# Performance work log

Hardware: AMD Instinct MI355X
Metric: run time of the kernel (lower is better)

## Reference

```python
import jax, jax.numpy as jnp
import numpy as np

EMBED_DIM = 528
NUM_HEADS = 8
HEAD_DIM = EMBED_DIM // NUM_HEADS  # 66


def setup_inputs() -> dict:
    key = jax.random.key(0)
    k1, k2, k3, k4, k5 = jax.random.split(key, 5)
    B, D, H, W, C = 1, 16, 16, 16, EMBED_DIM
    s = 1.0 / np.sqrt(C)
    return {
        "x": jax.random.normal(k1, (B, D, H, W, C), dtype=jnp.float32),
        "w_qkv": jax.random.uniform(k2, (3 * C, C), dtype=jnp.float32, minval=-s, maxval=s),
        "b_qkv": jax.random.uniform(k3, (3 * C,), dtype=jnp.float32, minval=-s, maxval=s),
        "w_proj": jax.random.uniform(k4, (C, C), dtype=jnp.float32, minval=-s, maxval=s),
        "b_proj": jax.random.uniform(k5, (C,), dtype=jnp.float32, minval=-s, maxval=s),
    }


def reference(x, w_qkv, b_qkv, w_proj, b_proj):
    B, D, H, W, C = x.shape
    N = D * H * W
    h, hd = NUM_HEADS, HEAD_DIM
    scaling = hd ** (-0.5)

    xt = x.reshape(B, N, C)
    # qkv projection: [B, N, 3C] -> [3, B, h, N, hd]
    qkv = xt @ w_qkv.T + b_qkv
    qkv = qkv.reshape(B, N, 3, h, hd).transpose(2, 0, 3, 1, 4)
    q, k, v = qkv[0], qkv[1], qkv[2]

    # full attention over all D*H*W tokens
    attn = jnp.einsum('bhqd,bhkd->bhqk', q, k) * scaling
    attn = jax.nn.softmax(attn, axis=-1)
    out = jnp.einsum('bhqk,bhkd->bhqd', attn, v)  # [B, h, N, hd]

    out = out.transpose(0, 2, 1, 3).reshape(B, N, h * hd)
    out = out @ w_proj.T + b_proj
    return out.reshape(B, D, H, W, C)
```

## Files before the change

### kernel.cpp

```cpp
#include <hip/hip_runtime.h>

typedef __attribute__((ext_vector_type(8))) short bf16x8;
typedef __attribute__((ext_vector_type(4))) float f32x4;
typedef __attribute__((ext_vector_type(16))) float f32x16;

#define DEV __device__ __forceinline__

static constexpr int N_TOK = 4096;
static constexpr int C     = 528;
static constexpr int NH    = 8;
static constexpr int HD    = 66;
static constexpr int HDP   = 96;
static constexpr int VD96  = 96;
static constexpr int KP    = 544;
static constexpr int NQKV  = 1584;
static constexpr int NQKVP = 1632;

DEV unsigned short f2bf(float f) {
    unsigned int u = __float_as_uint(f);
    u = (u + 0x7fffu + ((u >> 16) & 1u)) >> 16;
    return (unsigned short)u;
}
DEV float bf2f(unsigned short h) { return __uint_as_float(((unsigned int)h) << 16); }
DEV unsigned cvtpk2(float a, float b) {
    unsigned r;
    asm("v_cvt_pk_bf16_f32 %0, %1, %2" : "=v"(r) : "v"(a), "v"(b));
    return r;
}
DEV void plswap(unsigned &a, unsigned &b) {
    asm volatile("v_permlane32_swap_b32 %0, %1" : "+v"(a), "+v"(b));
}

__global__ void k_prep_all(const float* __restrict__ x, const float* __restrict__ w_qkv,
                           const float* __restrict__ w_proj,
                           unsigned short* __restrict__ xb, unsigned short* __restrict__ wqkvb,
                           unsigned short* __restrict__ whi, unsigned short* __restrict__ wlo,
                           unsigned short* __restrict__ qb, unsigned short* __restrict__ kbuf) {
    const int T0 = N_TOK * KP;
    const int T1 = T0 + NQKVP * KP;
    const int T2 = T1 + KP * KP;
    const int T3 = T2 + NH * N_TOK * (HDP - HD);
    for (int idx = blockIdx.x * 256 + threadIdx.x; idx < T3; idx += gridDim.x * 256) {
        if (idx < T0) {
            int n = idx / KP, k = idx - n * KP;
            xb[idx] = (k < C) ? f2bf(x[n * C + k]) : (unsigned short)0;
        } else if (idx < T1) {
            int j = idx - T0;
            int n = j / KP, k = j - n * KP;
            wqkvb[j] = (n < NQKV && k < C) ? f2bf(w_qkv[n * C + k]) : (unsigned short)0;
        } else if (idx < T2) {
            int j = idx - T1;
            int n = j / KP, k = j - n * KP;
            unsigned short hi = 0, lo = 0;
            if (n < C && k < C) {
                float v = w_proj[n * C + k];
                hi = f2bf(v);
                lo = f2bf(v - bf2f(hi));
            }
            whi[j] = hi; wlo[j] = lo;
        } else {
            int j = idx - T2;
            int n = j / 30, p = j - 30 * n;
            size_t a = (size_t)n * HDP + HD + p;
            qb[a] = 0; kbuf[a] = 0;
        }
    }
}

__launch_bounds__(256)
__global__ void k_gemm_qkv(const unsigned short* __restrict__ A,
                           const unsigned short* __restrict__ B,
                           const float* __restrict__ bias,
                           unsigned short* __restrict__ qb, unsigned short* __restrict__ kbuf,
                           unsigned short* __restrict__ vtmp) {
    constexpr int LDA = 40;
    __shared__ unsigned short Al[2][128 * LDA];
    __shared__ unsigned short Bl[2][96 * LDA];
    int tid = threadIdx.x, lane = tid & 63, wid = tid >> 6;
    int m0 = blockIdx.x * 128, n0 = blockIdx.y * 96;
    int wm = (wid >> 1) * 64, wn = (wid & 1) * 48;
    int arow0 = tid >> 2, arow1 = (256 + tid) >> 2, akc = (tid & 3) * 8;
    bool bhave = tid < 128;
    int brow1 = (256 + tid) >> 2;
    f32x4 acc[4][3] = {};
    bf16x8 ra0, ra1, rb0, rb1;

    ra0 = *(const bf16x8*)&A[(size_t)(m0 + arow0) * KP + akc];
    ra1 = *(const bf16x8*)&A[(size_t)(m0 + arow1) * KP + akc];
    rb0 = *(const bf16x8*)&B[(size_t)(n0 + arow0) * KP + akc];
    if (bhave) rb1 = *(const bf16x8*)&B[(size_t)(n0 + brow1) * KP + akc];
    *(bf16x8*)&Al[0][arow0 * LDA + akc] = ra0;
    *(bf16x8*)&Al[0][arow1 * LDA + akc] = ra1;
    *(bf16x8*)&Bl[0][arow0 * LDA + akc] = rb0;
    if (bhave) *(bf16x8*)&Bl[0][brow1 * LDA + akc] = rb1;
    __syncthreads();

    int kk = (lane >> 4) * 8, cc = lane & 15;
    for (int kt = 0; kt < 17; kt++) {
        int cur = kt & 1;
        if (kt < 16) {
            int k0 = (kt + 1) * 32;
            ra0 = *(const bf16x8*)&A[(size_t)(m0 + arow0) * KP + k0 + akc];
            ra1 = *(const bf16x8*)&A[(size_t)(m0 + arow1) * KP + k0 + akc];
            rb0 = *(const bf16x8*)&B[(size_t)(n0 + arow0) * KP + k0 + akc];
            if (bhave) rb1 = *(const bf16x8*)&B[(size_t)(n0 + brow1) * KP + k0 + akc];
        }
        bf16x8 af[4], bfr[3];
#pragma unroll
        for (int mi = 0; mi < 4; mi++) af[mi] = *(const bf16x8*)&Al[cur][(wm + mi * 16 + cc) * LDA + kk];
#pragma unroll
        for (int ni = 0; ni < 3; ni++) bfr[ni] = *(const bf16x8*)&Bl[cur][(wn + ni * 16 + cc) * LDA + kk];
#pragma unroll
        for (int mi = 0; mi < 4; mi++)
#pragma unroll
            for (int ni = 0; ni < 3; ni++)
                acc[mi][ni] = __builtin_amdgcn_mfma_f32_16x16x32_bf16(af[mi], bfr[ni], acc[mi][ni], 0, 0, 0);
        if (kt < 16) {
            int nxt = cur ^ 1;
            *(bf16x8*)&Al[nxt][arow0 * LDA + akc] = ra0;
            *(bf16x8*)&Al[nxt][arow1 * LDA + akc] = ra1;
            *(bf16x8*)&Bl[nxt][arow0 * LDA + akc] = rb0;
            if (bhave) *(bf16x8*)&Bl[nxt][brow1 * LDA + akc] = rb1;
        }
        __syncthreads();
    }
#pragma unroll
    for (int mi = 0; mi < 4; mi++)
#pragma unroll
        for (int ni = 0; ni < 3; ni++)
#pragma unroll
            for (int r = 0; r < 4; r++) {
                int row = m0 + wm + mi * 16 + (lane >> 4) * 4 + r;
                int col = n0 + wn + ni * 16 + cc;
                float v = acc[mi][ni][r] + (col < NQKV ? bias[col] : 0.f);
                unsigned short b = f2bf(v);
                if (col < 2 * C) {
                    int d5 = (col >= C) ? col - C : col;
                    unsigned h = (unsigned)d5 / 66u;
                    int dd = d5 - 66 * (int)h;
                    size_t a = ((size_t)h * N_TOK + row) * HDP + dd;
                    if (col >= C) kbuf[a] = b; else qb[a] = b;
                } else if (col < NQKV) {
                    vtmp[(size_t)row * C + (col - 2 * C)] = b;
                }
            }
}

__global__ void k_reshape_v(const unsigned short* __restrict__ vtmp, unsigned short* __restrict__ vt) {
    __shared__ unsigned short lt[64 * 104];
    int h = blockIdx.y, n0 = blockIdx.x * 64, tid = threadIdx.x;
#pragma unroll
    for (int i = 0; i < 24; i++) {
        int idx = i * 256 + tid;
        int ni = idx / 96, d = idx - ni * 96;
        unsigned short v = 0;
        if (d < HD) v = vtmp[(size_t)(n0 + ni) * C + h * HD + d];
        lt[ni * 104 + d] = v;
    }
    __syncthreads();
#pragma unroll
    for (int i = 0; i < 24; i++) {
        int idx = i * 256 + tid;
        int d = idx >> 6, ni = idx & 63;
        vt[((size_t)h * VD96 + d) * N_TOK + n0 + ni] = lt[ni * 104 + d];
    }
}

__launch_bounds__(512, 2)
__global__ void k_attn(const unsigned short* __restrict__ qb,
                       const unsigned short* __restrict__ kb,
                       const unsigned short* __restrict__ vt,
                       unsigned short* __restrict__ ahi,
                       unsigned short* __restrict__ alo) {
    __shared__ __align__(16) unsigned short S[128 * 128 + 96 * 128];
    int tid = threadIdx.x, lane = tid & 63, wid = tid >> 6;
    int wq = wid & 3;
    int kh = wid >> 2;
    int hi = lane >> 5, lq = lane & 31;
    int bid = blockIdx.x;
    int head = bid & 7;
    int q0 = (bid >> 3) * 128;
    const float SC2 = 0.12309149097933274f * 1.4426950408889634f;

    bf16x8 aq[6];
    {
        const unsigned short* qrow = qb + ((size_t)head * N_TOK + q0 + wq * 32 + lq) * HDP + hi * 8;
#pragma unroll
        for (int t = 0; t < 6; t++) aq[t] = *(const bf16x8*)&qrow[t * 16];
    }
    f32x16 o0 = {}, o1 = {}, o2 = {};
    float m_r = -3e38f, l_r = 0.f;

    const unsigned short* kg = kb + (size_t)head * N_TOK * HDP;
    const unsigned short* vg = vt + (size_t)head * VD96 * N_TOK;

    const unsigned short* gpK[3];
    const unsigned short* gpV[3];
    int laK[3], laV[3];
#pragma unroll
    for (int j = 0; j < 3; j++) {
        int c = j * 512 + tid;
        int row = c / 12, ch = c - row * 12;
        gpK[j] = kg + (size_t)row * HDP + ch * 8;
        laK[j] = row * 128 + ((ch ^ (row & 15)) << 3);
        int row2 = c >> 4, ch2 = c & 15;
        gpV[j] = vg + (size_t)row2 * N_TOK + ch2 * 8;
        laV[j] = 128 * 128 + row2 * 128 + ((ch2 ^ (row2 & 15)) << 3);
    }
#pragma unroll
    for (int j = 0; j < 3; j++) {
        *(bf16x8*)&S[laK[j]] = *(const bf16x8*)gpK[j];
        *(bf16x8*)&S[laV[j]] = *(const bf16x8*)gpV[j];
    }
    __syncthreads();

    for (int kt = 0; kt < 32; kt++) {
        bf16x8 gk[3], gv[3];
        if (kt < 31) {
            size_t n1 = (size_t)(kt + 1) * 128;
#pragma unroll
            for (int j = 0; j < 3; j++) {
                gk[j] = *(const bf16x8*)(gpK[j] + n1 * HDP);
                gv[j] = *(const bf16x8*)(gpV[j] + n1);
            }
        }

        f32x16 s0 = {}, s1 = {};
        {
            int r0 = kh * 64 + lq, r1 = r0 + 32;
#pragma unroll
            for (int t = 0; t < 6; t++) {
                bf16x8 ka0 = *(const bf16x8*)&S[r0 * 128 + (((2 * t + hi) ^ (r0 & 15)) << 3)];
                bf16x8 ka1 = *(const bf16x8*)&S[r1 * 128 + (((2 * t + hi) ^ (r1 & 15)) << 3)];
                s0 = __builtin_amdgcn_mfma_f32_32x32x16_bf16(ka0, aq[t], s0, 0, 0, 0);
                s1 = __builtin_amdgcn_mfma_f32_32x32x16_bf16(ka1, aq[t], s1, 0, 0, 0);
            }
        }

        float mx = s0[0];
#pragma unroll
        for (int r = 1; r < 16; r++) mx = fmaxf(mx, s0[r]);
#pragma unroll
        for (int r = 0; r < 16; r++) mx = fmaxf(mx, s1[r]);
        mx = fmaxf(mx, __shfl_xor(mx, 32, 64));
        if (!__all((mx - m_r) * SC2 <= 8.f)) {
            float mnew = fmaxf(m_r, mx);
            float fct = __builtin_amdgcn_exp2f((m_r - mnew) * SC2);
            m_r = mnew;
            l_r *= fct;
#pragma unroll
            for (int r = 0; r < 16; r++) { o0[r] *= fct; o1[r] *= fct; o2[r] *= fct; }
        }
        float nb = m_r * SC2;
        float lsum = 0.f;
#pragma unroll
        for (int r = 0; r < 16; r++) { s0[r] = __builtin_amdgcn_exp2f(__builtin_fmaf(s0[r], SC2, -nb)); lsum += s0[r]; }
#pragma unroll
        for (int r = 0; r < 16; r++) { s1[r] = __builtin_amdgcn_exp2f(__builtin_fmaf(s1[r], SC2, -nb)); lsum += s1[r]; }
        lsum += __shfl_xor(lsum, 32, 64);
        l_r += lsum;

        unsigned u0[2][4], u1[2][4];
#pragma unroll
        for (int a = 0; a < 4; a++) {
            u0[0][a] = cvtpk2(s0[4 * a + 0], s0[4 * a + 1]);
            u1[0][a] = cvtpk2(s0[4 * a + 2], s0[4 * a + 3]);
            u0[1][a] = cvtpk2(s1[4 * a + 0], s1[4 * a + 1]);
            u1[1][a] = cvtpk2(s1[4 * a + 2], s1[4 * a + 3]);
        }
#pragma unroll
        for (int kb2 = 0; kb2 < 2; kb2++)
#pragma unroll
            for (int a0 = 0; a0 < 4; a0 += 2) {
                plswap(u0[kb2][a0], u0[kb2][a0 + 1]);
                plswap(u1[kb2][a0], u1[kb2][a0 + 1]);
            }

#pragma unroll
        for (int t2 = 0; t2 < 4; t2++) {
            int kb2 = t2 >> 1, a0 = (t2 & 1) * 2;
            union { unsigned u[4]; bf16x8 v; } pf;
            pf.u[0] = u0[kb2][a0];     pf.u[1] = u1[kb2][a0];
            pf.u[2] = u0[kb2][a0 + 1]; pf.u[3] = u1[kb2][a0 + 1];
            int ch = kh * 8 + 2 * t2 + hi;
            int rv0 = lq, rv1 = 32 + lq, rv2 = 64 + lq;
            bf16x8 va0 = *(const bf16x8*)&S[128 * 128 + rv0 * 128 + ((ch ^ (rv0 & 15)) << 3)];
            bf16x8 va1 = *(const bf16x8*)&S[128 * 128 + rv1 * 128 + ((ch ^ (rv1 & 15)) << 3)];
            bf16x8 va2 = *(const bf16x8*)&S[128 * 128 + rv2 * 128 + ((ch ^ (rv2 & 15)) << 3)];
            o0 = __builtin_amdgcn_mfma_f32_32x32x16_bf16(va0, pf.v, o0, 0, 0, 0);
            o1 = __builtin_amdgcn_mfma_f32_32x32x16_bf16(va1, pf.v, o1, 0, 0, 0);
            o2 = __builtin_amdgcn_mfma_f32_32x32x16_bf16(va2, pf.v, o2, 0, 0, 0);
        }

        __syncthreads();
        if (kt < 31) {
#pragma unroll
            for (int j = 0; j < 3; j++) {
                *(bf16x8*)&S[laK[j]] = gk[j];
                *(bf16x8*)&S[laV[j]] = gv[j];
            }
        }
        __syncthreads();
    }

    float* xc = (float*)&S[0];
    float* rg = xc + (size_t)((wq * 64 + lane) * 52);
    if (kh == 1) {
#pragma unroll
        for (int r = 0; r < 16; r++) { rg[r] = o0[r]; rg[16 + r] = o1[r]; rg[32 + r] = o2[r]; }
        rg[48] = m_r; rg[49] = l_r;
    }
    __syncthreads();
    if (kh == 0) {
        float m1 = rg[48], l1 = rg[49];
        float m12 = fmaxf(m_r, m1);
        float f0 = __builtin_amdgcn_exp2f((m_r - m12) * SC2);
        float f1 = __builtin_amdgcn_exp2f((m1 - m12) * SC2);
        float inv = 1.f / (l_r * f0 + l1 * f1);
        int token = q0 + wq * 32 + lq;
#pragma unroll
        for (int db = 0; db < 3; db++) {
#pragma unroll
            for (int r = 0; r < 16; r++) {
                int d = db * 32 + (r & 3) + 8 * (r >> 2) + 4 * hi;
                if (d < HD) {
                    float own = (db == 0) ? o0[r] : (db == 1) ? o1[r] : o2[r];
                    float val = (own * f0 + rg[db * 16 + r] * f1) * inv;
                    unsigned short hb = f2bf(val);
                    float lo = val - bf2f(hb);
                    size_t a = (size_t)token * KP + head * HD + d;
                    ahi[a] = hb; alo[a] = f2bf(lo);
                }
            }
        }
    }
}

__launch_bounds__(256)
__global__ void k_gemm_proj(const unsigned short* __restrict__ Ahi_, const unsigned short* __restrict__ Alo_,
                            const unsigned short* __restrict__ Whi_, const unsigned short* __restrict__ Wlo_,
                            const float* __restrict__ bias, float* __restrict__ out) {
    constexpr int LDA = 40;
    __shared__ unsigned short Ah[2][128 * LDA], Aw[2][128 * LDA];
    __shared__ unsigned short Bh[2][64 * LDA],  Bw[2][64 * LDA];
    int tid = threadIdx.x, lane = tid & 63, wid = tid >> 6;
    int m0 = blockIdx.x * 128, n0 = blockIdx.y * 64;
    int wm = wid * 32;
    int arow0 = tid >> 2, arow1 = (256 + tid) >> 2, akc = (tid & 3) * 8;
    bool bok = (n0 + arow0) < KP;
    f32x4 acc[2][4] = {};
    bf16x8 rah0, rah1, ral0, ral1, rbh, rbl;
    const bf16x8 zero8 = {};

    rah0 = *(const bf16x8*)&Ahi_[(size_t)(m0 + arow0) * KP + akc];
    rah1 = *(const bf16x8*)&Ahi_[(size_t)(m0 + arow1) * KP + akc];
    ral0 = *(const bf16x8*)&Alo_[(size_t)(m0 + arow0) * KP + akc];
    ral1 = *(const bf16x8*)&Alo_[(size_t)(m0 + arow1) * KP + akc];
    rbh = bok ? *(const bf16x8*)&Whi_[(size_t)(n0 + arow0) * KP + akc] : zero8;
    rbl = bok ? *(const bf16x8*)&Wlo_[(size_t)(n0 + arow0) * KP + akc] : zero8;
    *(bf16x8*)&Ah[0][arow0 * LDA + akc] = rah0;
    *(bf16x8*)&Ah[0][arow1 * LDA + akc] = rah1;
    *(bf16x8*)&Aw[0][arow0 * LDA + akc] = ral0;
    *(bf16x8*)&Aw[0][arow1 * LDA + akc] = ral1;
    *(bf16x8*)&Bh[0][arow0 * LDA + akc] = rbh;
    *(bf16x8*)&Bw[0][arow0 * LDA + akc] = rbl;
    __syncthreads();

    int kk = (lane >> 4) * 8, cc = lane & 15;
    for (int kt = 0; kt < 17; kt++) {
        int cur = kt & 1;
        if (kt < 16) {
            int k0 = (kt + 1) * 32;
            rah0 = *(const bf16x8*)&Ahi_[(size_t)(m0 + arow0) * KP + k0 + akc];
            rah1 = *(const bf16x8*)&Ahi_[(size_t)(m0 + arow1) * KP + k0 + akc];
            ral0 = *(const bf16x8*)&Alo_[(size_t)(m0 + arow0) * KP + k0 + akc];
            ral1 = *(const bf16x8*)&Alo_[(size_t)(m0 + arow1) * KP + k0 + akc];
            rbh = bok ? *(const bf16x8*)&Whi_[(size_t)(n0 + arow0) * KP + k0 + akc] : zero8;
            rbl = bok ? *(const bf16x8*)&Wlo_[(size_t)(n0 + arow0) * KP + k0 + akc] : zero8;
        }
        bf16x8 ah[2], al[2], bh[4], bl[4];
#pragma unroll
        for (int mi = 0; mi < 2; mi++) {
            ah[mi] = *(const bf16x8*)&Ah[cur][(wm + mi * 16 + cc) * LDA + kk];
            al[mi] = *(const bf16x8*)&Aw[cur][(wm + mi * 16 + cc) * LDA + kk];
        }
#pragma unroll
        for (int ni = 0; ni < 4; ni++) {
            bh[ni] = *(const bf16x8*)&Bh[cur][(ni * 16 + cc) * LDA + kk];
            bl[ni] = *(const bf16x8*)&Bw[cur][(ni * 16 + cc) * LDA + kk];
        }
#pragma unroll
        for (int mi = 0; mi < 2; mi++)
#pragma unroll
            for (int ni = 0; ni < 4; ni++) {
                acc[mi][ni] = __builtin_amdgcn_mfma_f32_16x16x32_bf16(ah[mi], bh[ni], acc[mi][ni], 0, 0, 0);
                acc[mi][ni] = __builtin_amdgcn_mfma_f32_16x16x32_bf16(ah[mi], bl[ni], acc[mi][ni], 0, 0, 0);
                acc[mi][ni] = __builtin_amdgcn_mfma_f32_16x16x32_bf16(al[mi], bh[ni], acc[mi][ni], 0, 0, 0);
            }
        if (kt < 16) {
            int nxt = cur ^ 1;
            *(bf16x8*)&Ah[nxt][arow0 * LDA + akc] = rah0;
            *(bf16x8*)&Ah[nxt][arow1 * LDA + akc] = rah1;
            *(bf16x8*)&Aw[nxt][arow0 * LDA + akc] = ral0;
            *(bf16x8*)&Aw[nxt][arow1 * LDA + akc] = ral1;
            *(bf16x8*)&Bh[nxt][arow0 * LDA + akc] = rbh;
            *(bf16x8*)&Bw[nxt][arow0 * LDA + akc] = rbl;
        }
        __syncthreads();
    }
#pragma unroll
    for (int mi = 0; mi < 2; mi++)
#pragma unroll
        for (int ni = 0; ni < 4; ni++)
#pragma unroll
            for (int r = 0; r < 4; r++) {
                int row = m0 + wm + mi * 16 + (lane >> 4) * 4 + r;
                int col = n0 + ni * 16 + cc;
                if (col < C) out[(size_t)row * C + col] = acc[mi][ni][r] + bias[col];
            }
}

extern "C" void kernel_launch(void* const* d_in, const int* in_sizes, int n_in,
                              void* d_out, int out_size, void* d_ws, size_t ws_size,
                              hipStream_t stream) {
    const float* x      = (const float*)d_in[0];
    const float* w_qkv  = (const float*)d_in[1];
    const float* b_qkv  = (const float*)d_in[2];
    const float* w_proj = (const float*)d_in[3];
    const float* b_proj = (const float*)d_in[4];
    float* out = (float*)d_out;
    char* ws = (char*)d_ws;

    const size_t o_xb    = 0;
    const size_t o_wqkvb = o_xb    + 4456448;
    const size_t o_whi   = o_wqkvb + 1775616;
    const size_t o_wlo   = o_whi   + 591872;
    const size_t o_vtmp  = o_wlo   + 591872;
    const size_t o_qbf   = o_vtmp  + 4456448;
    const size_t o_kbf   = o_qbf   + 6291456;
    const size_t o_vt    = o_kbf   + 6291456;
    const size_t need    = o_vt + 6291456;
    if (ws_size < need) return;

    unsigned short* xb    = (unsigned short*)(ws + o_xb);
    unsigned short* wqkvb = (unsigned short*)(ws + o_wqkvb);
    unsigned short* whi   = (unsigned short*)(ws + o_whi);
    unsigned short* wlo   = (unsigned short*)(ws + o_wlo);
    unsigned short* vtmp  = (unsigned short*)(ws + o_vtmp);
    unsigned short* qbf   = (unsigned short*)(ws + o_qbf);
    unsigned short* kbf   = (unsigned short*)(ws + o_kbf);
    unsigned short* vt    = (unsigned short*)(ws + o_vt);
    unsigned short* ahi   = xb;
    unsigned short* alo   = vtmp;

    k_prep_all  <<<2048, 256, 0, stream>>>(x, w_qkv, w_proj, xb, wqkvb, whi, wlo, qbf, kbf);
    k_gemm_qkv  <<<dim3(N_TOK / 128, NQKVP / 96), 256, 0, stream>>>(xb, wqkvb, b_qkv, qbf, kbf, vtmp);
    k_reshape_v <<<dim3(N_TOK / 64, NH), 256, 0, stream>>>(vtmp, vt);
    k_attn      <<<dim3(256), 512, 0, stream>>>(qbf, kbf, vt, ahi, alo);
    k_gemm_proj <<<dim3(N_TOK / 128, 9), 256, 0, stream>>>(ahi, alo, whi, wlo, b_proj, out);
}
```

Before: 129.4 us.

## Double-buffer K/V tiles and split attention work four ways over keys

The attention kernel now gives each wave 64 queries (two 32-row groups) against a 32-key slice, so the 8 waves are 2 query groups by 4 key splits instead of 4 by 2. Each K and V fragment read from shared memory now feeds two MFMAs, which halves LDS reads per MFMA. K/V shared tiles are double-buffered, dropping one barrier per iteration, and s_setprio wraps the MFMA sections. The cost is more registers (launch bounds lowered to one block per SIMD group), double the LDS footprint, and a two-stage cross-wave reduction of the softmax partials at the end.

```diff
diff --git a/kernel.cpp b/kernel.cpp
--- a/kernel.cpp
+++ b/kernel.cpp
@@ -166,30 +166,33 @@
     }
 }
 
-__launch_bounds__(512, 2)
+__launch_bounds__(512, 1)
 __global__ void k_attn(const unsigned short* __restrict__ qb,
                        const unsigned short* __restrict__ kb,
                        const unsigned short* __restrict__ vt,
                        unsigned short* __restrict__ ahi,
                        unsigned short* __restrict__ alo) {
-    __shared__ __align__(16) unsigned short S[128 * 128 + 96 * 128];
+    __shared__ __align__(16) unsigned short Kl[2][128 * 128];
+    __shared__ __align__(16) unsigned short Vl[2][96 * 128];
     int tid = threadIdx.x, lane = tid & 63, wid = tid >> 6;
-    int wq = wid & 3;
-    int kh = wid >> 2;
+    int qsg = wid & 1;
+    int kh  = wid >> 1;
     int hi = lane >> 5, lq = lane & 31;
     int bid = blockIdx.x;
     int head = bid & 7;
     int q0 = (bid >> 3) * 128;
     const float SC2 = 0.12309149097933274f * 1.4426950408889634f;
 
-    bf16x8 aq[6];
+    bf16x8 aq0[6], aq1[6];
     {
-        const unsigned short* qrow = qb + ((size_t)head * N_TOK + q0 + wq * 32 + lq) * HDP + hi * 8;
-#pragma unroll
-        for (int t = 0; t < 6; t++) aq[t] = *(const bf16x8*)&qrow[t * 16];
-    }
-    f32x16 o0 = {}, o1 = {}, o2 = {};
-    float m_r = -3e38f, l_r = 0.f;
+        const unsigned short* qr0 = qb + ((size_t)head * N_TOK + q0 + qsg * 64 + lq) * HDP + hi * 8;
+        const unsigned short* qr1 = qr0 + 32 * HDP;
+#pragma unroll
+        for (int t = 0; t < 6; t++) { aq0[t] = *(const bf16x8*)&qr0[t * 16]; aq1[t] = *(const bf16x8*)&qr1[t * 16]; }
+    }
+    f32x16 o0a = {}, o0b = {}, o0c = {};
+    f32x16 o1a = {}, o1b = {}, o1c = {};
+    float m0r = -3e38f, l0r = 0.f, m1r = -3e38f, l1r = 0.f;
 
     const unsigned short* kg = kb + (size_t)head * N_TOK * HDP;
     const unsigned short* vg = vt + (size_t)head * VD96 * N_TOK;
@@ -205,16 +208,20 @@
         laK[j] = row * 128 + ((ch ^ (row & 15)) << 3);
         int row2 = c >> 4, ch2 = c & 15;
         gpV[j] = vg + (size_t)row2 * N_TOK + ch2 * 8;
-        laV[j] = 128 * 128 + row2 * 128 + ((ch2 ^ (row2 & 15)) << 3);
+        laV[j] = row2 * 128 + ((ch2 ^ (row2 & 15)) << 3);
     }
 #pragma unroll
     for (int j = 0; j < 3; j++) {
-        *(bf16x8*)&S[laK[j]] = *(const bf16x8*)gpK[j];
-        *(bf16x8*)&S[laV[j]] = *(const bf16x8*)gpV[j];
+        *(bf16x8*)&Kl[0][laK[j]] = *(const bf16x8*)gpK[j];
+        *(bf16x8*)&Vl[0][laV[j]] = *(const bf16x8*)gpV[j];
     }
     __syncthreads();
 
+    int rk = kh * 32 + lq;
+    int rv0 = lq, rv1 = 32 + lq, rv2 = 64 + lq;
+
     for (int kt = 0; kt < 32; kt++) {
+        int cur = kt & 1;
         bf16x8 gk[3], gv[3];
         if (kt < 31) {
             size_t n1 = (size_t)(kt + 1) * 128;
@@ -224,112 +231,180 @@
                 gv[j] = *(const bf16x8*)(gpV[j] + n1);
             }
         }
+        const unsigned short* Kc = &Kl[cur][0];
+        const unsigned short* Vc = &Vl[cur][0];
 
         f32x16 s0 = {}, s1 = {};
+        __builtin_amdgcn_s_setprio(1);
+#pragma unroll
+        for (int t = 0; t < 6; t++) {
+            bf16x8 ka = *(const bf16x8*)&Kc[rk * 128 + (((2 * t + hi) ^ (rk & 15)) << 3)];
+            s0 = __builtin_amdgcn_mfma_f32_32x32x16_bf16(ka, aq0[t], s0, 0, 0, 0);
+            s1 = __builtin_amdgcn_mfma_f32_32x32x16_bf16(ka, aq1[t], s1, 0, 0, 0);
+        }
+        __builtin_amdgcn_s_setprio(0);
+
         {
-            int r0 = kh * 64 + lq, r1 = r0 + 32;
-#pragma unroll
-            for (int t = 0; t < 6; t++) {
-                bf16x8 ka0 = *(const bf16x8*)&S[r0 * 128 + (((2 * t + hi) ^ (r0 & 15)) << 3)];
-                bf16x8 ka1 = *(const bf16x8*)&S[r1 * 128 + (((2 * t + hi) ^ (r1 & 15)) << 3)];
-                s0 = __builtin_amdgcn_mfma_f32_32x32x16_bf16(ka0, aq[t], s0, 0, 0, 0);
-                s1 = __builtin_amdgcn_mfma_f32_32x32x16_bf16(ka1, aq[t], s1, 0, 0, 0);
-            }
-        }
-
-        float mx = s0[0];
-#pragma unroll
-        for (int r = 1; r < 16; r++) mx = fmaxf(mx, s0[r]);
-#pragma unroll
-        for (int r = 0; r < 16; r++) mx = fmaxf(mx, s1[r]);
-        mx = fmaxf(mx, __shfl_xor(mx, 32, 64));
-        if (!__all((mx - m_r) * SC2 <= 8.f)) {
-            float mnew = fmaxf(m_r, mx);
-            float fct = __builtin_amdgcn_exp2f((m_r - mnew) * SC2);
-            m_r = mnew;
-            l_r *= fct;
-#pragma unroll
-            for (int r = 0; r < 16; r++) { o0[r] *= fct; o1[r] *= fct; o2[r] *= fct; }
-        }
-        float nb = m_r * SC2;
-        float lsum = 0.f;
-#pragma unroll
-        for (int r = 0; r < 16; r++) { s0[r] = __builtin_amdgcn_exp2f(__builtin_fmaf(s0[r], SC2, -nb)); lsum += s0[r]; }
-#pragma unroll
-        for (int r = 0; r < 16; r++) { s1[r] = __builtin_amdgcn_exp2f(__builtin_fmaf(s1[r], SC2, -nb)); lsum += s1[r]; }
-        lsum += __shfl_xor(lsum, 32, 64);
-        l_r += lsum;
-
-        unsigned u0[2][4], u1[2][4];
+            float mx = s0[0];
+#pragma unroll
+            for (int r = 1; r < 16; r++) mx = fmaxf(mx, s0[r]);
+            mx = fmaxf(mx, __shfl_xor(mx, 32, 64));
+            if (!__all((mx - m0r) * SC2 <= 8.f)) {
+                float mnew = fmaxf(m0r, mx);
+                float fct = __builtin_amdgcn_exp2f((m0r - mnew) * SC2);
+                m0r = mnew; l0r *= fct;
+#pragma unroll
+                for (int r = 0; r < 16; r++) { o0a[r] *= fct; o0b[r] *= fct; o0c[r] *= fct; }
+            }
+            float nb = m0r * SC2, lsum = 0.f;
+#pragma unroll
+            for (int r = 0; r < 16; r++) { s0[r] = __builtin_amdgcn_exp2f(__builtin_fmaf(s0[r], SC2, -nb)); lsum += s0[r]; }
+            lsum += __shfl_xor(lsum, 32, 64);
+            l0r += lsum;
+        }
+        {
+            float mx = s1[0];
+#pragma unroll
+            for (int r = 1; r < 16; r++) mx = fmaxf(mx, s1[r]);
+            mx = fmaxf(mx, __shfl_xor(mx, 32, 64));
+            if (!__all((mx - m1r) * SC2 <= 8.f)) {
+                float mnew = fmaxf(m1r, mx);
+                float fct = __builtin_amdgcn_exp2f((m1r - mnew) * SC2);
+                m1r = mnew; l1r *= fct;
+#pragma unroll
+                for (int r = 0; r < 16; r++) { o1a[r] *= fct; o1b[r] *= fct; o1c[r] *= fct; }
+            }
+            float nb = m1r * SC2, lsum = 0.f;
+#pragma unroll
+            for (int r = 0; r < 16; r++) { s1[r] = __builtin_amdgcn_exp2f(__builtin_fmaf(s1[r], SC2, -nb)); lsum += s1[r]; }
+            lsum += __shfl_xor(lsum, 32, 64);
+            l1r += lsum;
+        }
+
+        unsigned u00[4], u01[4], u10[4], u11[4];
 #pragma unroll
         for (int a = 0; a < 4; a++) {
-            u0[0][a] = cvtpk2(s0[4 * a + 0], s0[4 * a + 1]);
-            u1[0][a] = cvtpk2(s0[4 * a + 2], s0[4 * a + 3]);
-            u0[1][a] = cvtpk2(s1[4 * a + 0], s1[4 * a + 1]);
-            u1[1][a] = cvtpk2(s1[4 * a + 2], s1[4 * a + 3]);
-        }
-#pragma unroll
-        for (int kb2 = 0; kb2 < 2; kb2++)
-#pragma unroll
-            for (int a0 = 0; a0 < 4; a0 += 2) {
-                plswap(u0[kb2][a0], u0[kb2][a0 + 1]);
-                plswap(u1[kb2][a0], u1[kb2][a0 + 1]);
-            }
-
-#pragma unroll
-        for (int t2 = 0; t2 < 4; t2++) {
-            int kb2 = t2 >> 1, a0 = (t2 & 1) * 2;
-            union { unsigned u[4]; bf16x8 v; } pf;
-            pf.u[0] = u0[kb2][a0];     pf.u[1] = u1[kb2][a0];
-            pf.u[2] = u0[kb2][a0 + 1]; pf.u[3] = u1[kb2][a0 + 1];
-            int ch = kh * 8 + 2 * t2 + hi;
-            int rv0 = lq, rv1 = 32 + lq, rv2 = 64 + lq;
-            bf16x8 va0 = *(const bf16x8*)&S[128 * 128 + rv0 * 128 + ((ch ^ (rv0 & 15)) << 3)];
-            bf16x8 va1 = *(const bf16x8*)&S[128 * 128 + rv1 * 128 + ((ch ^ (rv1 & 15)) << 3)];
-            bf16x8 va2 = *(const bf16x8*)&S[128 * 128 + rv2 * 128 + ((ch ^ (rv2 & 15)) << 3)];
-            o0 = __builtin_amdgcn_mfma_f32_32x32x16_bf16(va0, pf.v, o0, 0, 0, 0);
-            o1 = __builtin_amdgcn_mfma_f32_32x32x16_bf16(va1, pf.v, o1, 0, 0, 0);
-            o2 = __builtin_amdgcn_mfma_f32_32x32x16_bf16(va2, pf.v, o2, 0, 0, 0);
-        }
-
+            u00[a] = cvtpk2(s0[4 * a + 0], s0[4 * a + 1]);
+            u01[a] = cvtpk2(s0[4 * a + 2], s0[4 * a + 3]);
+            u10[a] = cvtpk2(s1[4 * a + 0], s1[4 * a + 1]);
+            u11[a] = cvtpk2(s1[4 * a + 2], s1[4 * a + 3]);
+        }
+        plswap(u00[0], u00[1]); plswap(u00[2], u00[3]);
+        plswap(u01[0], u01[1]); plswap(u01[2], u01[3]);
+        plswap(u10[0], u10[1]); plswap(u10[2], u10[3]);
+        plswap(u11[0], u11[1]); plswap(u11[2], u11[3]);
+
+        __builtin_amdgcn_s_setprio(1);
+#pragma unroll
+        for (int t2 = 0; t2 < 2; t2++) {
+            int a0 = t2 * 2;
+            union { unsigned u[4]; bf16x8 v; } p0, p1;
+            p0.u[0] = u00[a0]; p0.u[1] = u01[a0]; p0.u[2] = u00[a0 + 1]; p0.u[3] = u01[a0 + 1];
+            p1.u[0] = u10[a0]; p1.u[1] = u11[a0]; p1.u[2] = u10[a0 + 1]; p1.u[3] = u11[a0 + 1];
+            int ch = kh * 4 + 2 * t2 + hi;
+            bf16x8 va0 = *(const bf16x8*)&Vc[rv0 * 128 + ((ch ^ (rv0 & 15)) << 3)];
+            bf16x8 va1 = *(const bf16x8*)&Vc[rv1 * 128 + ((ch ^ (rv1 & 15)) << 3)];
+            bf16x8 va2 = *(const bf16x8*)&Vc[rv2 * 128 + ((ch ^ (rv2 & 15)) << 3)];
+            o0a = __builtin_amdgcn_mfma_f32_32x32x16_bf16(va0, p0.v, o0a, 0, 0, 0);
+            o1a = __builtin_amdgcn_mfma_f32_32x32x16_bf16(va0, p1.v, o1a, 0, 0, 0);
+            o0b = __builtin_amdgcn_mfma_f32_32x32x16_bf16(va1, p0.v, o0b, 0, 0, 0);
+            o1b = __builtin_amdgcn_mfma_f32_32x32x16_bf16(va1, p1.v, o1b, 0, 0, 0);
+            o0c = __builtin_amdgcn_mfma_f32_32x32x16_bf16(va2, p0.v, o0c, 0, 0, 0);
+            o1c = __builtin_amdgcn_mfma_f32_32x32x16_bf16(va2, p1.v, o1c, 0, 0, 0);
+        }
+        __builtin_amdgcn_s_setprio(0);
+
+        if (kt < 31) {
+            int nxt = cur ^ 1;
+#pragma unroll
+            for (int j = 0; j < 3; j++) {
+                *(bf16x8*)&Kl[nxt][laK[j]] = gk[j];
+                *(bf16x8*)&Vl[nxt][laV[j]] = gv[j];
+            }
+        }
         __syncthreads();
-        if (kt < 31) {
-#pragma unroll
-            for (int j = 0; j < 3; j++) {
-                *(bf16x8*)&S[laK[j]] = gk[j];
-                *(bf16x8*)&S[laV[j]] = gv[j];
-            }
+    }
+
+    float* xc = (float*)&Kl[0][0];
+    {
+        int slot = qsg * 2 + (kh & 1);
+        float* rg0 = xc + (size_t)(((slot * 64 + lane) * 2 + 0) * 50);
+        float* rg1 = xc + (size_t)(((slot * 64 + lane) * 2 + 1) * 50);
+        if (kh >= 2) {
+#pragma unroll
+            for (int r = 0; r < 16; r++) {
+                rg0[r] = o0a[r]; rg0[16 + r] = o0b[r]; rg0[32 + r] = o0c[r];
+                rg1[r] = o1a[r]; rg1[16 + r] = o1b[r]; rg1[32 + r] = o1c[r];
+            }
+            rg0[48] = m0r; rg0[49] = l0r; rg1[48] = m1r; rg1[49] = l1r;
         }
         __syncthreads();
-    }
-
-    float* xc = (float*)&S[0];
-    float* rg = xc + (size_t)((wq * 64 + lane) * 52);
-    if (kh == 1) {
-#pragma unroll
-        for (int r = 0; r < 16; r++) { rg[r] = o0[r]; rg[16 + r] = o1[r]; rg[32 + r] = o2[r]; }
-        rg[48] = m_r; rg[49] = l_r;
-    }
-    __syncthreads();
-    if (kh == 0) {
-        float m1 = rg[48], l1 = rg[49];
-        float m12 = fmaxf(m_r, m1);
-        float f0 = __builtin_amdgcn_exp2f((m_r - m12) * SC2);
-        float f1 = __builtin_amdgcn_exp2f((m1 - m12) * SC2);
-        float inv = 1.f / (l_r * f0 + l1 * f1);
-        int token = q0 + wq * 32 + lq;
-#pragma unroll
-        for (int db = 0; db < 3; db++) {
+        if (kh < 2) {
+            float mo = rg0[48], lo = rg0[49];
+            float mm = fmaxf(m0r, mo);
+            float f0 = __builtin_amdgcn_exp2f((m0r - mm) * SC2);
+            float f1 = __builtin_amdgcn_exp2f((mo - mm) * SC2);
+            l0r = l0r * f0 + lo * f1; m0r = mm;
 #pragma unroll
             for (int r = 0; r < 16; r++) {
-                int d = db * 32 + (r & 3) + 8 * (r >> 2) + 4 * hi;
-                if (d < HD) {
-                    float own = (db == 0) ? o0[r] : (db == 1) ? o1[r] : o2[r];
-                    float val = (own * f0 + rg[db * 16 + r] * f1) * inv;
-                    unsigned short hb = f2bf(val);
-                    float lo = val - bf2f(hb);
-                    size_t a = (size_t)token * KP + head * HD + d;
-                    ahi[a] = hb; alo[a] = f2bf(lo);
+                o0a[r] = o0a[r] * f0 + rg0[r] * f1;
+                o0b[r] = o0b[r] * f0 + rg0[16 + r] * f1;
+                o0c[r] = o0c[r] * f0 + rg0[32 + r] * f1;
+            }
+            mo = rg1[48]; lo = rg1[49];
+            mm = fmaxf(m1r, mo);
+            f0 = __builtin_amdgcn_exp2f((m1r - mm) * SC2);
+            f1 = __builtin_amdgcn_exp2f((mo - mm) * SC2);
+            l1r = l1r * f0 + lo * f1; m1r = mm;
+#pragma unroll
+            for (int r = 0; r < 16; r++) {
+                o1a[r] = o1a[r] * f0 + rg1[r] * f1;
+                o1b[r] = o1b[r] * f0 + rg1[16 + r] * f1;
+                o1c[r] = o1c[r] * f0 + rg1[32 + r] * f1;
+            }
+        }
+        __syncthreads();
+    }
+    {
+        float* rg0 = xc + (size_t)(((qsg * 64 + lane) * 2 + 0) * 50);
+        float* rg1 = xc + (size_t)(((qsg * 64 + lane) * 2 + 1) * 50);
+        if (kh == 1) {
+#pragma unroll
+            for (int r = 0; r < 16; r++) {
+                rg0[r] = o0a[r]; rg0[16 + r] = o0b[r]; rg0[32 + r] = o0c[r];
+                rg1[r] = o1a[r]; rg1[16 + r] = o1b[r]; rg1[32 + r] = o1c[r];
+            }
+            rg0[48] = m0r; rg0[49] = l0r; rg1[48] = m1r; rg1[49] = l1r;
+        }
+        __syncthreads();
+        if (kh == 0) {
+#pragma unroll
+            for (int qg = 0; qg < 2; qg++) {
+                float* rg = qg ? rg1 : rg0;
+                float mr = qg ? m1r : m0r;
+                float lr = qg ? l1r : l0r;
+                float mo = rg[48], lo = rg[49];
+                float mm = fmaxf(mr, mo);
+                float f0 = __builtin_amdgcn_exp2f((mr - mm) * SC2);
+                float f1 = __builtin_amdgcn_exp2f((mo - mm) * SC2);
+                float inv = 1.f / (lr * f0 + lo * f1);
+                int token = q0 + qsg * 64 + qg * 32 + lq;
+#pragma unroll
+                for (int db = 0; db < 3; db++) {
+#pragma unroll
+                    for (int r = 0; r < 16; r++) {
+                        int d = db * 32 + (r & 3) + 8 * (r >> 2) + 4 * hi;
+                        if (d < HD) {
+                            float own;
+                            if (qg == 0) own = (db == 0) ? o0a[r] : (db == 1) ? o0b[r] : o0c[r];
+                            else         own = (db == 0) ? o1a[r] : (db == 1) ? o1b[r] : o1c[r];
+                            float val = (own * f0 + rg[db * 16 + r] * f1) * inv;
+                            unsigned short hb = f2bf(val);
+                            float lov = val - bf2f(hb);
+                            size_t a = (size_t)token * KP + head * HD + d;
+                            ahi[a] = hb; alo[a] = f2bf(lov);
+                        }
+                    }
                 }
             }
         }
```

Result: no change. 130.3 us (+0.7%).
